# Optimization experiments

Hardware: AMD Instinct MI355X
Metric: run time of the kernel (lower is better)

The kernel has to match this reference:

```python
import jax, jax.numpy as jnp
import numpy as np

B, L, E, H, K = 128, 512, 512, 256, 64


def setup_inputs() -> dict:
    key = jax.random.key(0)
    ks = jax.random.split(key, 13)
    s = 1.0 / np.sqrt(H)

    def u(k, shape):
        return jax.random.uniform(k, shape, jnp.float32, -s, s)

    return {
        "input_batch": jax.random.normal(ks[0], (B, L, E), jnp.float32),
        "labels": jax.random.randint(ks[1], (B, L), 0, K),
        "w_ih_f": u(ks[2], (4 * H, E)),
        "w_hh_f": u(ks[3], (4 * H, H)),
        "b_ih_f": u(ks[4], (4 * H,)),
        "b_hh_f": u(ks[5], (4 * H,)),
        "w_ih_b": u(ks[6], (4 * H, E)),
        "w_hh_b": u(ks[7], (4 * H, H)),
        "b_ih_b": u(ks[8], (4 * H,)),
        "b_hh_b": u(ks[9], (4 * H,)),
        "w_emit": u(ks[10], (K, 2 * H)),
        "b_emit": jnp.zeros((K,), jnp.float32),
        "transition": jax.random.normal(ks[11], (K, K), jnp.float32),
    }


def _lstm_dir(x, w_ih, w_hh, b_ih, b_hh):
    """One LSTM direction. x: (L,B,E) -> hidden states (L,B,H). PyTorch gate order i,f,g,o."""
    Hh = w_hh.shape[1]
    # input contribution for all timesteps at once: (L,B,4H)
    pre = jnp.einsum('lbe,ge->lbg', x, w_ih) + b_ih + b_hh

    def step(carry, p_t):
        h, c = carry
        g = p_t + h @ w_hh.T  # (B,4H)
        i, f, gg, o = jnp.split(g, 4, axis=-1)
        c = jax.nn.sigmoid(f) * c + jax.nn.sigmoid(i) * jnp.tanh(gg)
        h = jax.nn.sigmoid(o) * jnp.tanh(c)
        return (h, c), h

    init = (jnp.zeros((x.shape[1], Hh), x.dtype), jnp.zeros((x.shape[1], Hh), x.dtype))
    _, hs = jax.lax.scan(step, init, pre)
    return hs


def _bilstm_crf_loss(input_batch, labels, w_ih_f, w_hh_f, b_ih_f, b_hh_f,
                     w_ih_b, w_hh_b, b_ih_b, b_hh_b, w_emit, b_emit, transition):
    x = jnp.transpose(input_batch, (1, 0, 2))  # (L,B,E)
    h_f = _lstm_dir(x, w_ih_f, w_hh_f, b_ih_f, b_hh_f)
    h_b = _lstm_dir(x[::-1], w_ih_b, w_hh_b, b_ih_b, b_hh_b)[::-1]
    h = jnp.concatenate([h_f, h_b], axis=-1)  # (L,B,2H)
    emit = jnp.einsum('lbh,kh->b018'.replace('018', 'lk'), h, w_emit) + b_emit  # placeholder fixed below
    emit = jnp.einsum('lbh,kh->lbk', h, w_emit) + b_emit  # (L,B,K)
    emit = jnp.transpose(emit, (1, 0, 2))  # (B,L,K)

    # gold path score
    gold_emit = jnp.take_along_axis(emit, labels[:, :, None], axis=2)[:, :, 0]  # (B,L)
    gold_trans = transition[labels[:, :-1], labels[:, 1:]]  # (B,L-1)
    total_score = gold_emit.sum(axis=1) + gold_trans.sum(axis=1)  # (B,)

    # CRF forward algorithm (log partition), scan over timesteps 1..L-1
    def crf_step(d, e_t):
        # d: (B,K) log alpha; e_t: (B,K) emit at step t
        d = jax.nn.logsumexp(d[:, :, None] + transition[None, :, :] + e_t[:, None, :], axis=1)
        return d, None

    d0 = emit[:, 0]  # (B,K)
    dT, _ = jax.lax.scan(crf_step, d0, jnp.transpose(emit[:, 1:], (1, 0, 2)))
    log_z = jax.nn.logsumexp(dT, axis=1)  # (B,)
    return -(total_score - log_z)  # (B,)


def reference(input_batch, labels, w_ih_f, w_hh_f, b_ih_f, b_hh_f,
              w_ih_b, w_hh_b, b_ih_b, b_hh_b, w_emit, b_emit, transition):
    return _bilstm_crf_loss(input_batch, labels, w_ih_f, w_hh_f, b_ih_f, b_hh_f,
                            w_ih_b, w_hh_b, b_ih_b, b_hh_b, w_emit, b_emit, transition)
```

## Files before the change

### kernel.cpp

```cpp
#include <hip/hip_runtime.h>
#include <hip/hip_bf16.h>

#define B_   128
#define L_   512
#define E_   512
#define H_   256
#define K_   64
#define G4H  1024
#define LOG2E 1.4426950408889634f

typedef __bf16 bf16x8 __attribute__((ext_vector_type(8)));
typedef float  f32x4  __attribute__((ext_vector_type(4)));
typedef int    i32x8  __attribute__((ext_vector_type(8)));

__device__ inline unsigned short f2bf(float f) {
    unsigned int x = __builtin_bit_cast(unsigned int, f);
    unsigned int r = (x + 0x7fffu + ((x >> 16) & 1u)) >> 16;
    return (unsigned short)r;
}
__device__ inline float bf2f(unsigned short u) {
    unsigned int x = ((unsigned int)u) << 16;
    return __builtin_bit_cast(float, x);
}
__device__ inline unsigned int pack2(float lo, float hi) {
    return (unsigned int)f2bf(lo) | ((unsigned int)f2bf(hi) << 16);
}
__device__ inline float ex2(float x) { return __builtin_amdgcn_exp2f(x); }
__device__ inline float rcp_(float x) { return __builtin_amdgcn_rcpf(x); }

__device__ inline void gl_lds16(const unsigned short* g, unsigned short* l) {
    __builtin_amdgcn_global_load_lds(
        (const __attribute__((address_space(1))) unsigned int*)g,
        (__attribute__((address_space(3))) unsigned int*)l, 16, 0, 0);
}

__global__ void setup_convert(const float* __restrict__ whh_f, const float* __restrict__ whh_b,
                              const float* __restrict__ wemit,
                              const float* __restrict__ wihf, const float* __restrict__ wihb,
                              const float* __restrict__ bihf, const float* __restrict__ bhhf,
                              const float* __restrict__ bihb, const float* __restrict__ bhhb,
                              unsigned char* __restrict__ whh8,
                              unsigned short* __restrict__ wemit_bf,
                              unsigned short* __restrict__ wp,
                              float* __restrict__ bias_p) {
    int i = blockIdx.x * 256 + threadIdx.x;
    if (i < 262144) {
        int j = 2 * i;
        float v0 = (j < 262144) ? whh_f[j] : whh_b[j - 262144];
        float v1 = (j + 1 < 262144) ? whh_f[j + 1] : whh_b[j + 1 - 262144];
        int pk = __builtin_amdgcn_cvt_pk_fp8_f32(v0 * LOG2E, v1 * LOG2E, 0, false);
        ((unsigned short*)whh8)[i] = (unsigned short)(pk & 0xffff);
    }
    if (i < K_ * 2 * H_) wemit_bf[i] = f2bf(wemit[i]);
    if (i < 131072) {
        int rp = i >> 6;
        int k8 = (i & 63) * 8;
        int dd = rp >> 10, np = rp & 1023;
        int srow = (np & 3) * 256 + (np >> 2);
        const float* src = (dd == 0 ? wihf : wihb) + (size_t)srow * 512 + k8;
        float4 a  = *reinterpret_cast<const float4*>(src);
        float4 b2 = *reinterpret_cast<const float4*>(src + 4);
        uint4 pk = { pack2(a.x * LOG2E, a.y * LOG2E), pack2(a.z * LOG2E, a.w * LOG2E),
                     pack2(b2.x * LOG2E, b2.y * LOG2E), pack2(b2.z * LOG2E, b2.w * LOG2E) };
        *reinterpret_cast<uint4*>(wp + (size_t)rp * 512 + k8) = pk;
    }
    if (i < 2048) {
        int dd = i >> 10, np = i & 1023;
        int srow = (np & 3) * 256 + (np >> 2);
        bias_p[i] = ((dd == 0) ? (bihf[srow] + bhhf[srow]) : (bihb[srow] + bhhb[srow])) * LOG2E;
    }
}

__global__ void convert_x(const float* __restrict__ x, unsigned short* __restrict__ xb) {
    int i = blockIdx.x * 256 + threadIdx.x;
    float4 a = reinterpret_cast<const float4*>(x)[i * 2];
    float4 b = reinterpret_cast<const float4*>(x)[i * 2 + 1];
    uint4 p = { pack2(a.x, a.y), pack2(a.z, a.w), pack2(b.x, b.y), pack2(b.z, b.w) };
    reinterpret_cast<uint4*>(xb)[i] = p;
}

__global__ __launch_bounds__(256) void pre_gemm(
    const unsigned short* __restrict__ xb,
    const unsigned short* __restrict__ wp,
    const float* __restrict__ bias_p,
    unsigned short* __restrict__ pre3)
{
    __shared__ unsigned short A_lds[128 * 32];
    __shared__ unsigned short B_lds[128 * 32];

    int nt = blockIdx.x, mt = blockIdx.y;
    int tid = threadIdx.x;
    int n0 = nt * 128;
    int b  = mt >> 2, l0 = (mt & 3) * 128;
    int w = tid >> 6, lane = tid & 63;
    int q = lane >> 4, ln = lane & 15;
    int wm = (w >> 1) * 64, wn = (w & 1) * 64;

    f32x4 acc[4][4];
    #pragma unroll
    for (int i = 0; i < 4; ++i)
        #pragma unroll
        for (int j = 0; j < 4; ++j) acc[i][j] = (f32x4){0.f, 0.f, 0.f, 0.f};

    int r_ = tid >> 2, kp = (tid & 3) * 8;
    const unsigned short* asrc0 = xb + ((size_t)b * 512 + l0 + r_) * 512 + kp;
    const unsigned short* asrc1 = asrc0 + (size_t)64 * 512;
    const unsigned short* bsrc0 = wp + (size_t)(n0 + r_) * 512 + kp;
    const unsigned short* bsrc1 = bsrc0 + (size_t)64 * 512;
    unsigned short* adst0 = &A_lds[tid * 8];
    unsigned short* adst1 = &A_lds[2048 + tid * 8];
    unsigned short* bdst0 = &B_lds[tid * 8];
    unsigned short* bdst1 = &B_lds[2048 + tid * 8];

    for (int kc = 0; kc < 16; ++kc) {
        int k0 = kc * 32;
        gl_lds16(asrc0 + k0, adst0);
        gl_lds16(asrc1 + k0, adst1);
        gl_lds16(bsrc0 + k0, bdst0);
        gl_lds16(bsrc1 + k0, bdst1);
        __syncthreads();

        bf16x8 af[4], bfv[4];
        #pragma unroll
        for (int ms = 0; ms < 4; ++ms)
            af[ms] = *reinterpret_cast<const bf16x8*>(&A_lds[(wm + ms * 16 + ln) * 32 + q * 8]);
        #pragma unroll
        for (int ns = 0; ns < 4; ++ns)
            bfv[ns] = *reinterpret_cast<const bf16x8*>(&B_lds[(wn + ns * 16 + ln) * 32 + q * 8]);
        #pragma unroll
        for (int ms = 0; ms < 4; ++ms)
            #pragma unroll
            for (int ns = 0; ns < 4; ++ns)
                acc[ms][ns] = __builtin_amdgcn_mfma_f32_16x16x32_bf16(af[ms], bfv[ns], acc[ms][ns], 0, 0, 0);
        __syncthreads();
    }

    #pragma unroll
    for (int ns = 0; ns < 4; ++ns) {
        int n = n0 + wn + ns * 16 + ln;
        float bias = bias_p[n];
        int dsel = n >> 10, np = n & 1023;
        #pragma unroll
        for (int ms = 0; ms < 4; ++ms) {
            #pragma unroll
            for (int rg = 0; rg < 4; ++rg) {
                int l = l0 + wm + ms * 16 + q * 4 + rg;
                pre3[(((size_t)dsel * 128 + b) * 512 + l) * 1024 + np] = f2bf(acc[ms][ns][rg] + bias);
            }
        }
    }
}

__global__ __launch_bounds__(512, 2) void lstm_scan(
    const unsigned short* __restrict__ pre3,
    const unsigned char* __restrict__ whh8,
    unsigned short* __restrict__ hcat)
{
    __shared__ unsigned char h_lds[2][16 * 272];

    int wg = blockIdx.x;
    int d = wg >> 7, b = wg & 127;
    int tid = threadIdx.x, w = tid >> 6, lane = tid & 63;
    int q = lane >> 4, ln = lane & 15;

    const unsigned char* whh_d = whh8 + (size_t)d * (1024 * 256);
    const unsigned short* pre_wg = pre3 + ((size_t)d * 128 + b) * (512 * 1024);

    i32x8 wh[4][2][2];
    #pragma unroll
    for (int g = 0; g < 4; ++g)
        #pragma unroll
        for (int s = 0; s < 2; ++s) {
            int row = g * 256 + (w + 8 * s) * 16 + ln;
            #pragma unroll
            for (int kc = 0; kc < 2; ++kc)
                wh[g][s][kc] = *reinterpret_cast<const i32x8*>(
                    whh_d + (size_t)row * 256 + kc * 128 + q * 32);
        }

    for (int i = tid; i < (2 * 16 * 272) / 4; i += 512) ((int*)h_lds)[i] = 0;

    bool act = (lane < 32);
    int s_  = (lane >> 4) & 1;
    int col = (w + 8 * s_) * 16 + ln;

    ushort4 p0 = {0,0,0,0}, p1 = {0,0,0,0};
    if (act) {
        int la  = (d == 0) ? 0 : (L_ - 1);
        int lb_ = (d == 0) ? 1 : (L_ - 2);
        p0 = *reinterpret_cast<const ushort4*>(pre_wg + (size_t)la * 1024 + col * 4);
        p1 = *reinterpret_cast<const ushort4*>(pre_wg + (size_t)lb_ * 1024 + col * 4);
    }
    __syncthreads();

    float cst = 0.f;

    for (int t = 0; t < L_; ++t) {
        int p = t & 1;
        int l = (d == 0) ? t : (L_ - 1 - t);

        ushort4 p2 = {0,0,0,0};
        if (act) {
            int t2 = (t + 2 < L_) ? (t + 2) : (L_ - 1);
            int l2 = (d == 0) ? t2 : (L_ - 1 - t2);
            p2 = *reinterpret_cast<const ushort4*>(pre_wg + (size_t)l2 * 1024 + col * 4);
        }

        f32x4 acc[4][2];
        #pragma unroll
        for (int g = 0; g < 4; ++g) {
            acc[g][0] = (f32x4){0.f, 0.f, 0.f, 0.f};
            acc[g][1] = (f32x4){0.f, 0.f, 0.f, 0.f};
        }
        __builtin_amdgcn_s_setprio(1);
        #pragma unroll
        for (int kc = 0; kc < 2; ++kc) {
            const unsigned char* ab = &h_lds[p][ln * 272 + kc * 128 + q * 32];
            uint4 a0 = *reinterpret_cast<const uint4*>(ab);
            uint4 a1 = *reinterpret_cast<const uint4*>(ab + 16);
            i32x8 af = { (int)a0.x, (int)a0.y, (int)a0.z, (int)a0.w,
                         (int)a1.x, (int)a1.y, (int)a1.z, (int)a1.w };
            #pragma unroll
            for (int g = 0; g < 4; ++g)
                #pragma unroll
                for (int s = 0; s < 2; ++s)
                    acc[g][s] = __builtin_amdgcn_mfma_scale_f32_16x16x128_f8f6f4(
                        af, wh[g][s][kc], acc[g][s], 0, 0,
                        0, 0x7f7f7f7f, 0, 0x7f7f7f7f);
        }
        __builtin_amdgcn_s_setprio(0);

        float gv[4];
        #pragma unroll
        for (int g = 0; g < 4; ++g) {
            float lo = __shfl(acc[g][0][0], ln);
            float hi = __shfl(acc[g][1][0], ln);
            gv[g] = s_ ? hi : lo;
        }

        if (act) {
            float vi = gv[0] + bf2f(p0.x);
            float vf = gv[1] + bf2f(p0.y);
            float vg = gv[2] + bf2f(p0.z);
            float vo = gv[3] + bf2f(p0.w);
            float ei  = ex2(vi);
            float e2g = ex2(vg + vg);
            float itg = (ei * (e2g - 1.f)) * rcp_((1.f + ei) * (1.f + e2g));
            float sf  = rcp_(1.f + ex2(-vf));
            float cn  = fmaf(sf, cst, itg);
            cst = cn;
            float tc  = fmaf(-2.f, rcp_(1.f + ex2((2.f * LOG2E) * cn)), 1.f);
            float so  = rcp_(1.f + ex2(-vo));
            float hn  = so * tc;
            int pk = __builtin_amdgcn_cvt_pk_fp8_f32(hn, hn, 0, false);
            h_lds[p ^ 1][col] = (unsigned char)(pk & 0xff);
            hcat[((size_t)l * 128 + b) * 512 + d * 256 + col] = f2bf(hn);
        }
        asm volatile("s_waitcnt lgkmcnt(0)" ::: "memory");
        __builtin_amdgcn_s_barrier();

        p0 = p1; p1 = p2;
    }
}

__global__ __launch_bounds__(256) void emit_gemm(
    const unsigned short* __restrict__ hcat,
    const unsigned short* __restrict__ wemit,
    const float* __restrict__ bemit,
    float* __restrict__ emit)
{
    int m0 = blockIdx.x * 64;
    int tid = threadIdx.x, w = tid >> 6, lane = tid & 63;
    int quad = lane >> 4, ln = lane & 15;
    int mrow = m0 + w * 16;

    f32x4 acc[4];
    #pragma unroll
    for (int i = 0; i < 4; ++i) acc[i] = (f32x4){0.f, 0.f, 0.f, 0.f};

    const unsigned short* arow = hcat + (size_t)(mrow + ln) * 512;
    #pragma unroll 4
    for (int kc = 0; kc < 16; ++kc) {
        bf16x8 af = *reinterpret_cast<const bf16x8*>(arow + kc * 32 + quad * 8);
        #pragma unroll
        for (int T = 0; T < 4; ++T) {
            bf16x8 bfv = *reinterpret_cast<const bf16x8*>(wemit + (size_t)(T * 16 + ln) * 512 + kc * 32 + quad * 8);
            acc[T] = __builtin_amdgcn_mfma_f32_16x16x32_bf16(af, bfv, acc[T], 0, 0, 0);
        }
    }
    #pragma unroll
    for (int T = 0; T < 4; ++T) {
        int k = T * 16 + ln;
        float bias = bemit[k];
        #pragma unroll
        for (int rg = 0; rg < 4; ++rg) {
            int m = mrow + quad * 4 + rg;
            int ll = m >> 7, bidx = m & 127;
            emit[((size_t)bidx * L_ + ll) * K_ + k] = acc[T][rg] + bias;
        }
    }
}

__global__ __launch_bounds__(64) void crf_kernel(
    const float* __restrict__ emit,
    const int* __restrict__ labels,
    const float* __restrict__ trans,
    float* __restrict__ out)
{
    __shared__ float els[2][64];
    int b = blockIdx.x, lane = threadIdx.x;
    const float* eb = emit + (size_t)b * L_ * K_;
    const int* lb = labels + (size_t)b * L_;

    float gold = 0.f;
    for (int t = lane; t < L_; t += 64) gold += eb[(size_t)t * K_ + lb[t]];
    for (int t = lane; t < L_ - 1; t += 64) gold += trans[lb[t] * K_ + lb[t + 1]];
    #pragma unroll
    for (int off = 32; off; off >>= 1) gold += __shfl_down(gold, off);

    float expT[64];
    #pragma unroll
    for (int i = 0; i < 64; ++i) expT[i] = __expf(trans[i * K_ + lane]);

    float dstate = eb[lane];
    float enext = eb[K_ + lane];
    for (int t = 1; t < L_; ++t) {
        float ecur = enext;
        if (t + 1 < L_) enext = eb[(size_t)(t + 1) * K_ + lane];
        float M = __builtin_amdgcn_readfirstlane(dstate);
        float e = __expf(dstate - M);
        float* el = els[t & 1];
        el[lane] = e;
        asm volatile("s_waitcnt lgkmcnt(0)" ::: "memory");
        float s0 = 0.f, s1 = 0.f, s2 = 0.f, s3 = 0.f;
        #pragma unroll
        for (int i = 0; i < 64; i += 16) {
            float4 a0 = *reinterpret_cast<const float4*>(&el[i]);
            float4 a1 = *reinterpret_cast<const float4*>(&el[i + 4]);
            float4 a2 = *reinterpret_cast<const float4*>(&el[i + 8]);
            float4 a3 = *reinterpret_cast<const float4*>(&el[i + 12]);
            s0 = fmaf(a0.x, expT[i], s0);      s0 = fmaf(a0.y, expT[i + 1], s0);
            s0 = fmaf(a0.z, expT[i + 2], s0);  s0 = fmaf(a0.w, expT[i + 3], s0);
            s1 = fmaf(a1.x, expT[i + 4], s1);  s1 = fmaf(a1.y, expT[i + 5], s1);
            s1 = fmaf(a1.z, expT[i + 6], s1);  s1 = fmaf(a1.w, expT[i + 7], s1);
            s2 = fmaf(a2.x, expT[i + 8], s2);  s2 = fmaf(a2.y, expT[i + 9], s2);
            s2 = fmaf(a2.z, expT[i + 10], s2); s2 = fmaf(a2.w, expT[i + 11], s2);
            s3 = fmaf(a3.x, expT[i + 12], s3); s3 = fmaf(a3.y, expT[i + 13], s3);
            s3 = fmaf(a3.z, expT[i + 14], s3); s3 = fmaf(a3.w, expT[i + 15], s3);
        }
        dstate = M + __logf((s0 + s1) + (s2 + s3)) + ecur;
    }
    float M = __builtin_amdgcn_readfirstlane(dstate);
    float e = __expf(dstate - M);
    float s = e;
    #pragma unroll
    for (int off = 32; off; off >>= 1) s += __shfl_xor(s, off);
    float logZ = M + __logf(s);
    if (lane == 0) out[b] = -(gold - logZ);
}

#define OFF_PRE    ((size_t)0)
#define OFF_EMIT   OFF_PRE
#define OFF_HCAT   ((size_t)268435456)
#define OFF_XB     OFF_HCAT
#define OFF_WHH8   ((size_t)(OFF_HCAT + 67108864))
#define OFF_WEMIT  ((size_t)(OFF_WHH8 + 524288))
#define OFF_WP     ((size_t)(OFF_WEMIT + 65536))
#define OFF_BIAS   ((size_t)(OFF_WP + 2097152))

extern "C" void kernel_launch(void* const* d_in, const int* in_sizes, int n_in,
                              void* d_out, int out_size, void* d_ws, size_t ws_size,
                              hipStream_t stream) {
    const float* x      = (const float*)d_in[0];
    const int*   labels = (const int*)d_in[1];
    const float* wihf   = (const float*)d_in[2];
    const float* whhf   = (const float*)d_in[3];
    const float* bihf   = (const float*)d_in[4];
    const float* bhhf   = (const float*)d_in[5];
    const float* wihb   = (const float*)d_in[6];
    const float* whhb   = (const float*)d_in[7];
    const float* bihb   = (const float*)d_in[8];
    const float* bhhb   = (const float*)d_in[9];
    const float* wemit  = (const float*)d_in[10];
    const float* bemit  = (const float*)d_in[11];
    const float* trans  = (const float*)d_in[12];
    float* out = (float*)d_out;

    char* ws = (char*)d_ws;
    unsigned short* pre3   = (unsigned short*)(ws + OFF_PRE);
    unsigned short* hcat   = (unsigned short*)(ws + OFF_HCAT);
    unsigned short* xb     = (unsigned short*)(ws + OFF_XB);
    float*          emit   = (float*)(ws + OFF_EMIT);
    unsigned char*  whh8   = (unsigned char*)(ws + OFF_WHH8);
    unsigned short* we_bf  = (unsigned short*)(ws + OFF_WEMIT);
    unsigned short* wp     = (unsigned short*)(ws + OFF_WP);
    float*          bias_p = (float*)(ws + OFF_BIAS);

    setup_convert<<<1024, 256, 0, stream>>>(whhf, whhb, wemit, wihf, wihb,
                                            bihf, bhhf, bihb, bhhb,
                                            whh8, we_bf, wp, bias_p);
    convert_x<<<16384, 256, 0, stream>>>(x, xb);
    pre_gemm<<<dim3(16, 512), 256, 0, stream>>>(xb, wp, bias_p, pre3);
    lstm_scan<<<256, 512, 0, stream>>>(pre3, whh8, hcat);
    emit_gemm<<<1024, 256, 0, stream>>>(hcat, we_bf, bemit, emit);
    crf_kernel<<<128, 64, 0, stream>>>(emit, labels, trans, out);
}
```

Baseline: 1.120 ms.

## Shrink h LDS buffer to a single row and reorder MFMAs to overlap shuffles

```diff
diff --git a/kernel.cpp b/kernel.cpp
--- a/kernel.cpp
+++ b/kernel.cpp
@@ -156,7 +156,7 @@
     const unsigned char* __restrict__ whh8,
     unsigned short* __restrict__ hcat)
 {
-    __shared__ unsigned char h_lds[2][16 * 272];
+    __shared__ unsigned char h_lds[2][256];
 
     int wg = blockIdx.x;
     int d = wg >> 7, b = wg & 127;
@@ -178,7 +178,7 @@
                     whh_d + (size_t)row * 256 + kc * 128 + q * 32);
         }
 
-    for (int i = tid; i < (2 * 16 * 272) / 4; i += 512) ((int*)h_lds)[i] = 0;
+    if (tid < 128) ((int*)h_lds)[tid] = 0;
 
     bool act = (lane < 32);
     int s_  = (lane >> 4) & 1;
@@ -206,43 +206,51 @@
             p2 = *reinterpret_cast<const ushort4*>(pre_wg + (size_t)l2 * 1024 + col * 4);
         }
 
+        const unsigned char* hb = h_lds[p];
+        uint4 a00 = *reinterpret_cast<const uint4*>(hb + q * 32);
+        uint4 a01 = *reinterpret_cast<const uint4*>(hb + q * 32 + 16);
+        uint4 a10 = *reinterpret_cast<const uint4*>(hb + 128 + q * 32);
+        uint4 a11 = *reinterpret_cast<const uint4*>(hb + 128 + q * 32 + 16);
+        i32x8 af0 = { (int)a00.x, (int)a00.y, (int)a00.z, (int)a00.w,
+                      (int)a01.x, (int)a01.y, (int)a01.z, (int)a01.w };
+        i32x8 af1 = { (int)a10.x, (int)a10.y, (int)a10.z, (int)a10.w,
+                      (int)a11.x, (int)a11.y, (int)a11.z, (int)a11.w };
+
         f32x4 acc[4][2];
         #pragma unroll
         for (int g = 0; g < 4; ++g) {
             acc[g][0] = (f32x4){0.f, 0.f, 0.f, 0.f};
             acc[g][1] = (f32x4){0.f, 0.f, 0.f, 0.f};
         }
-        __builtin_amdgcn_s_setprio(1);
-        #pragma unroll
-        for (int kc = 0; kc < 2; ++kc) {
-            const unsigned char* ab = &h_lds[p][ln * 272 + kc * 128 + q * 32];
-            uint4 a0 = *reinterpret_cast<const uint4*>(ab);
-            uint4 a1 = *reinterpret_cast<const uint4*>(ab + 16);
-            i32x8 af = { (int)a0.x, (int)a0.y, (int)a0.z, (int)a0.w,
-                         (int)a1.x, (int)a1.y, (int)a1.z, (int)a1.w };
-            #pragma unroll
-            for (int g = 0; g < 4; ++g)
-                #pragma unroll
-                for (int s = 0; s < 2; ++s)
-                    acc[g][s] = __builtin_amdgcn_mfma_scale_f32_16x16x128_f8f6f4(
-                        af, wh[g][s][kc], acc[g][s], 0, 0,
-                        0, 0x7f7f7f7f, 0, 0x7f7f7f7f);
-        }
-        __builtin_amdgcn_s_setprio(0);
-
-        float gv[4];
-        #pragma unroll
-        for (int g = 0; g < 4; ++g) {
-            float lo = __shfl(acc[g][0][0], ln);
-            float hi = __shfl(acc[g][1][0], ln);
-            gv[g] = s_ ? hi : lo;
-        }
+        #pragma unroll
+        for (int g = 0; g < 4; ++g)
+            acc[g][0] = __builtin_amdgcn_mfma_scale_f32_16x16x128_f8f6f4(
+                af0, wh[g][0][0], acc[g][0], 0, 0, 0, 0x7f7f7f7f, 0, 0x7f7f7f7f);
+        #pragma unroll
+        for (int g = 0; g < 4; ++g)
+            acc[g][0] = __builtin_amdgcn_mfma_scale_f32_16x16x128_f8f6f4(
+                af1, wh[g][0][1], acc[g][0], 0, 0, 0, 0x7f7f7f7f, 0, 0x7f7f7f7f);
+        float lo[4];
+        #pragma unroll
+        for (int g = 0; g < 4; ++g) lo[g] = __shfl(acc[g][0][0], ln);
+        __builtin_amdgcn_sched_barrier(0);
+        #pragma unroll
+        for (int g = 0; g < 4; ++g)
+            acc[g][1] = __builtin_amdgcn_mfma_scale_f32_16x16x128_f8f6f4(
+                af0, wh[g][1][0], acc[g][1], 0, 0, 0, 0x7f7f7f7f, 0, 0x7f7f7f7f);
+        #pragma unroll
+        for (int g = 0; g < 4; ++g)
+            acc[g][1] = __builtin_amdgcn_mfma_scale_f32_16x16x128_f8f6f4(
+                af1, wh[g][1][1], acc[g][1], 0, 0, 0, 0x7f7f7f7f, 0, 0x7f7f7f7f);
+        float hi[4];
+        #pragma unroll
+        for (int g = 0; g < 4; ++g) hi[g] = __shfl(acc[g][1][0], ln);
 
         if (act) {
-            float vi = gv[0] + bf2f(p0.x);
-            float vf = gv[1] + bf2f(p0.y);
-            float vg = gv[2] + bf2f(p0.z);
-            float vo = gv[3] + bf2f(p0.w);
+            float vi = (s_ ? hi[0] : lo[0]) + bf2f(p0.x);
+            float vf = (s_ ? hi[1] : lo[1]) + bf2f(p0.y);
+            float vg = (s_ ? hi[2] : lo[2]) + bf2f(p0.z);
+            float vo = (s_ ? hi[3] : lo[3]) + bf2f(p0.w);
             float ei  = ex2(vi);
             float e2g = ex2(vg + vg);
             float itg = (ei * (e2g - 1.f)) * rcp_((1.f + ei) * (1.f + e2g));
@@ -256,8 +264,7 @@
             h_lds[p ^ 1][col] = (unsigned char)(pk & 0xff);
             hcat[((size_t)l * 128 + b) * 512 + d * 256 + col] = f2bf(hn);
         }
-        asm volatile("s_waitcnt lgkmcnt(0)" ::: "memory");
-        __builtin_amdgcn_s_barrier();
+        __syncthreads();
 
         p0 = p1; p1 = p2;
     }
```

Measured after the change: 1.107 ms. No clear change (-1.1%).
